# Performance work log

Hardware: AMD Instinct MI355X
Metric: run time of the kernel (lower is better)

## Reference

```python
import jax, jax.numpy as jnp
import numpy as np
from jax import lax

B, C, H, W = 32, 684, 16, 64
HID, A, CK, K = 256, 512, 512, 11


def setup_inputs() -> dict:
    key = jax.random.key(0)
    ks = jax.random.split(key, 12)
    s = 0.02
    return {
        "cnn_features": jax.random.normal(ks[0], (B, C, H, W), jnp.float32),
        "hidden": jax.random.normal(ks[1], (B, HID), jnp.float32),
        "alpha_sum": jax.random.uniform(ks[2], (B, 1, H, W), jnp.float32),
        "image_mask": jnp.ones((B, 1, H, W), jnp.float32),
        # hidden_weight: Linear(HID -> A)
        "Wh": jax.random.normal(ks[3], (A, HID), jnp.float32) * s,
        "bh": jnp.zeros((A,), jnp.float32),
        # encoder_feature_conv: Conv2d(C -> A, 1x1) == pointwise linear
        "Wec": jax.random.normal(ks[4], (A, C), jnp.float32) * s,
        "bec": jnp.zeros((A,), jnp.float32),
        # attention_conv: Conv2d(1 -> CK, 11x11, pad 5, no bias)
        "Wac": jax.random.normal(ks[5], (CK, 1, K, K), jnp.float32) * s,
        # attention_weight: Linear(CK -> A, no bias)
        "Waw": jax.random.normal(ks[6], (A, CK), jnp.float32) * s,
        # alpha_convert: Linear(A -> 1)
        "Wv": jax.random.normal(ks[7], (1, A), jnp.float32) * s,
        "bv": jnp.zeros((1,), jnp.float32),
    }


def reference(cnn_features, hidden, alpha_sum, image_mask,
              Wh, bh, Wec, bec, Wac, Waw, Wv, bv):
    # query = hidden_weight(hidden): [B, A]
    query = hidden @ Wh.T + bh
    # attention_conv(alpha_sum): [B, CK, H, W]
    ast = lax.conv_general_dilated(
        alpha_sum, Wac, window_strides=(1, 1),
        padding=[(K // 2, K // 2), (K // 2, K // 2)],
        dimension_numbers=("NCHW", "OIHW", "NCHW"))
    # attention_weight on permuted conv output: [B, H, W, A]
    coverage_alpha = jnp.einsum("bkhw,ak->bhwa", ast, Waw)
    # encoder_feature_conv (1x1 conv == pointwise linear): [B, H, W, A]
    cnn_trans = jnp.einsum("bchw,ac->bhwa", cnn_features, Wec) + bec
    # additive attention score
    alpha_score = jnp.tanh(query[:, None, None, :] + coverage_alpha + cnn_trans)
    # alpha_convert -> scalar energy per position: [B, H, W]
    energy = jnp.einsum("bhwa,a->bhw", alpha_score, Wv[0]) + bv[0]
    energy = energy - energy.max()  # global max-subtract as in original
    energy_exp = jnp.exp(energy) * image_mask[:, 0]
    denom = energy_exp.sum(axis=(-1, -2))[:, None, None] + 1e-10
    alpha = energy_exp / denom  # [B, H, W]
    alpha_sum_new = alpha[:, None, :, :] + alpha_sum  # [B, 1, H, W]
    # context: weighted spatial sum over features -> [B, C]
    context_vector = jnp.einsum("bhw,bchw->bc", alpha, cnn_features)
    return (context_vector, alpha, alpha_sum_new)
```

## Files before the change

kernel.cpp:

```cpp
#include <hip/hip_runtime.h>
#include <hip/hip_bf16.h>
#include <math.h>

#define Bn   32
#define Cn   684
#define Hn   16
#define Wn   64
#define HWn  1024
#define HIDn 256
#define An   512
#define KKn  121
#define CREAL 805
#define CPAD 832
#define NSTEP 26
#define NBLK 256

#define OUT_ALPHA 21888
#define OUT_ASUM  (21888 + 32768)

typedef short short8 __attribute__((ext_vector_type(8)));
typedef float floatx4 __attribute__((ext_vector_type(4)));

__device__ __forceinline__ unsigned short f2bf(float f) {
    union { float f; unsigned int i; } v; v.f = f;
    unsigned int i = v.i;
    return (unsigned short)((i + 0x7fffu + ((i >> 16) & 1u)) >> 16);
}
__device__ __forceinline__ unsigned int cvt2(float lo, float hi) {
    __hip_bfloat162 h = __float22bfloat162_rn(float2{lo, hi});
    union { __hip_bfloat162 h; unsigned int u; } cv; cv.h = h;
    return cv.u;
}

__device__ __forceinline__ size_t bfr_idx(int n, int k) {
    return ((((size_t)(n >> 4) * 26 + (k >> 5)) * 64
             + ((k >> 3) & 3) * 16 + (n & 15)) * 8) + (k & 7);
}

__global__ __launch_bounds__(256) void k_prep(
    const float* __restrict__ hidden,
    const float* __restrict__ Wh,
    const float* __restrict__ bh,
    const float* __restrict__ bec,
    const float* __restrict__ Wec,
    const float* __restrict__ Wac,
    const float* __restrict__ Waw,
    float* __restrict__ query,
    unsigned short* __restrict__ Bfr,
    float* __restrict__ energy)
{
    __shared__ float sbuf[512];
    const int blk = blockIdx.x, t = threadIdx.x;
    if (blk < 512) {
        const int a = blk;
        sbuf[t]       = Waw[(size_t)a * 512 + t];
        sbuf[t + 256] = Waw[(size_t)a * 512 + t + 256];
        __syncthreads();
        for (int cp = t; cp < Cn; cp += 256)
            Bfr[bfr_idx(a, cp)] = f2bf(Wec[(size_t)a * Cn + cp]);
        if (t < KKn) {
            float s = 0.f;
            #pragma unroll 8
            for (int k = 0; k < 512; ++k)
                s = fmaf(sbuf[k], Wac[k * KKn + t], s);
            Bfr[bfr_idx(a, Cn + t)] = f2bf(s);
        }
        for (int cp = CREAL + t; cp < CPAD; cp += 256)
            Bfr[bfr_idx(a, cp)] = 0;
    } else if (blk < 544) {
        const int b = blk - 512;
        sbuf[t] = (t < HIDn) ? hidden[b * HIDn + t] : 0.f;
        __syncthreads();
        for (int a = t; a < An; a += 256) {
            const float4* wp = (const float4*)(Wh + (size_t)a * HIDn);
            float s = bh[a] + bec[a];
            #pragma unroll 8
            for (int i = 0; i < HIDn / 4; ++i) {
                float4 w = wp[i];
                s = fmaf(sbuf[4 * i],     w.x, s);
                s = fmaf(sbuf[4 * i + 1], w.y, s);
                s = fmaf(sbuf[4 * i + 2], w.z, s);
                s = fmaf(sbuf[4 * i + 3], w.w, s);
            }
            query[b * An + a] = s;
        }
    } else {
        const int b = blk - 544;
        #pragma unroll
        for (int i = 0; i < 4; ++i)
            energy[b * HWn + i * 256 + t] = 0.f;
    }
}

__global__ __launch_bounds__(512, 4) void k_energy(
    const float* __restrict__ X,
    const float* __restrict__ asum,
    const float* __restrict__ Wv,
    const float* __restrict__ query,
    const unsigned short* __restrict__ Bfr,
    float* __restrict__ energy)
{
    __shared__ __align__(16) unsigned short As[2][64 * 40];
    __shared__ float plane[878];
    __shared__ int   lut[148];
    __shared__ float qs[NBLK];
    __shared__ float wvs[NBLK];
    __shared__ float red[8][64];

    const int t = threadIdx.x;
    const int d = blockIdx.x;
    const int nh  = (d >> 3) & 1;
    const int pid = (d >> 4) * 8 + (d & 7);
    const int hh = pid & 15, b = pid >> 4;
    const int w = t >> 6, lane = t & 63;
    const int q = lane >> 4, r = lane & 15;
    const int nbase = nh * NBLK;
    const int mA = lane;

    const float* Xb = X + (size_t)b * Cn * HWn + hh * Wn;
    const unsigned short* Bp = Bfr + (size_t)(nh * 16 + w * 2) * 26 * 512;

    for (int i = t; i < 878; i += 512) {
        float v = 0.f;
        if (i < 814) {
            int di = i / 74, cc = i - di * 74;
            int h2 = hh + di - 5, w2 = cc - 5;
            if (h2 >= 0 && h2 < Hn && w2 >= 0 && w2 < Wn)
                v = asum[b * HWn + h2 * Wn + w2];
        }
        plane[i] = v;
    }
    if (t < 148) {
        int off = 814;
        if (t < 121) { int di = t / 11; off = di * 74 + (t - di * 11); }
        lut[t] = off;
    }
    if (t < NBLK) {
        qs[t]  = query[b * An + nbase + t];
        wvs[t] = Wv[nbase + t];
    }
    {
        const float* xp = Xb + (size_t)(w * 4) * HWn + mA;
        float v0 = xp[0];
        float v1 = xp[(size_t)1 * HWn];
        float v2 = xp[(size_t)2 * HWn];
        float v3 = xp[(size_t)3 * HWn];
        *(uint2*)&As[0][mA * 40 + w * 4] = make_uint2(cvt2(v0, v1), cvt2(v2, v3));
    }
    __syncthreads();

    floatx4 acc[4][2];
    #pragma unroll
    for (int mf = 0; mf < 4; ++mf)
        #pragma unroll
        for (int nf = 0; nf < 2; ++nf)
            acc[mf][nf] = (floatx4){0.f, 0.f, 0.f, 0.f};

    for (int ch = 0; ch < NSTEP; ++ch) {
        const int cur = ch & 1;

        short8 bf[2];
        #pragma unroll
        for (int nf = 0; nf < 2; ++nf)
            bf[nf] = *(const short8*)(Bp + ((size_t)(nf * 26 + ch)) * 512 + lane * 8);

        short8 af[4];
        #pragma unroll
        for (int mf = 0; mf < 4; ++mf)
            af[mf] = *(const short8*)&As[cur][(mf * 16 + r) * 40 + q * 8];

        if (ch < NSTEP - 1) {
            const int c0 = (ch + 1) * 32 + w * 4;
            float va[4];
            #pragma unroll
            for (int j = 0; j < 4; ++j) {
                const int row = c0 + j;
                if (row < Cn) va[j] = Xb[(size_t)row * HWn + mA];
                else          va[j] = plane[lut[row - Cn] + mA];
            }
            *(uint2*)&As[cur ^ 1][mA * 40 + w * 4] =
                make_uint2(cvt2(va[0], va[1]), cvt2(va[2], va[3]));
        }

        #pragma unroll
        for (int mf = 0; mf < 4; ++mf)
            #pragma unroll
            for (int nf = 0; nf < 2; ++nf)
                acc[mf][nf] = __builtin_amdgcn_mfma_f32_16x16x32_bf16(
                    af[mf], bf[nf], acc[mf][nf], 0, 0, 0);

        __syncthreads();
    }

    float ep[16];
    #pragma unroll
    for (int i = 0; i < 16; ++i) ep[i] = 0.f;
    #pragma unroll
    for (int nf = 0; nf < 2; ++nf) {
        int nl = w * 32 + nf * 16 + r;
        float qv = qs[nl], wv = wvs[nl];
        #pragma unroll
        for (int mf = 0; mf < 4; ++mf)
            #pragma unroll
            for (int rg = 0; rg < 4; ++rg) {
                float x = acc[mf][nf][rg] + qv;
                float e2 = __expf(2.f * x);
                float th = 1.f - 2.f * __builtin_amdgcn_rcpf(e2 + 1.f);
                ep[mf * 4 + rg] += wv * th;
            }
    }
    #pragma unroll
    for (int i = 0; i < 16; ++i) {
        #pragma unroll
        for (int msk = 1; msk <= 8; msk <<= 1)
            ep[i] += __shfl_xor(ep[i], msk, 64);
    }
    if (r == 0) {
        #pragma unroll
        for (int mf = 0; mf < 4; ++mf)
            #pragma unroll
            for (int rg = 0; rg < 4; ++rg)
                red[w][mf * 16 + q * 4 + rg] = ep[mf * 4 + rg];
    }
    __syncthreads();
    if (t < 64) {
        float s = 0.f;
        #pragma unroll
        for (int ww = 0; ww < 8; ++ww) s += red[ww][t];
        atomicAdd(&energy[b * HWn + hh * Wn + t], s);
    }
}

__global__ __launch_bounds__(256) void k_softmax(
    const float* __restrict__ mask,
    const float* __restrict__ asum,
    float* __restrict__ energy,
    float* __restrict__ out)
{
    __shared__ float rsm[8];
    const int b = blockIdx.x;
    const int t = threadIdx.x, lane = t & 63, wid = t >> 6;

    float e[4], ex[4];
    #pragma unroll
    for (int i = 0; i < 4; ++i) e[i] = energy[b * HWn + i * 256 + t];
    float m = fmaxf(fmaxf(e[0], e[1]), fmaxf(e[2], e[3]));
    for (int off = 32; off >= 1; off >>= 1) m = fmaxf(m, __shfl_down(m, off, 64));
    if (lane == 0) rsm[wid] = m;
    __syncthreads();
    if (t == 0)
        rsm[4] = fmaxf(fmaxf(rsm[0], rsm[1]), fmaxf(rsm[2], rsm[3]));
    __syncthreads();
    const float M = rsm[4];
    float s = 0.f;
    #pragma unroll
    for (int i = 0; i < 4; ++i) {
        ex[i] = expf(e[i] - M) * mask[b * HWn + i * 256 + t];
        s += ex[i];
    }
    for (int off = 32; off >= 1; off >>= 1) s += __shfl_down(s, off, 64);
    __syncthreads();
    if (lane == 0) rsm[wid] = s;
    __syncthreads();
    if (t == 0) rsm[5] = rsm[0] + rsm[1] + rsm[2] + rsm[3] + 1e-10f;
    __syncthreads();
    const float denom = rsm[5];
    #pragma unroll
    for (int i = 0; i < 4; ++i) {
        int p = i * 256 + t;
        float a = ex[i] / denom;
        energy[b * HWn + p] = a;
        out[OUT_ALPHA + b * HWn + p] = a;
        out[OUT_ASUM  + b * HWn + p] = a + asum[b * HWn + p];
    }
}

__global__ __launch_bounds__(256) void k_ctx(
    const float* __restrict__ X,
    const float* __restrict__ alpha,
    float* __restrict__ out)
{
    __shared__ float al[1024];
    const int bx = blockIdx.x, b = blockIdx.y;
    const int t = threadIdx.x, lane = t & 63, wid = t >> 6;

    #pragma unroll
    for (int i = 0; i < 4; ++i) al[i * 256 + t] = alpha[b * HWn + i * 256 + t];
    __syncthreads();

    const int c = bx * 4 + wid;
    const float* xp = X + ((size_t)(b * Cn + c)) * HWn;
    float s2 = 0.f;
    #pragma unroll
    for (int i = 0; i < 4; ++i) {
        int off = i * 256 + lane * 4;
        float4 x = *(const float4*)(xp + off);
        float4 a = *(const float4*)(al + off);
        s2 = fmaf(a.x, x.x, s2);
        s2 = fmaf(a.y, x.y, s2);
        s2 = fmaf(a.z, x.z, s2);
        s2 = fmaf(a.w, x.w, s2);
    }
    for (int off = 32; off >= 1; off >>= 1) s2 += __shfl_down(s2, off, 64);
    if (lane == 0) out[b * Cn + c] = s2;
}

extern "C" void kernel_launch(void* const* d_in, const int* in_sizes, int n_in,
                              void* d_out, int out_size, void* d_ws, size_t ws_size,
                              hipStream_t stream)
{
    const float* X      = (const float*)d_in[0];
    const float* hidden = (const float*)d_in[1];
    const float* asum   = (const float*)d_in[2];
    const float* mask   = (const float*)d_in[3];
    const float* Wh     = (const float*)d_in[4];
    const float* bh     = (const float*)d_in[5];
    const float* Wec    = (const float*)d_in[6];
    const float* bec    = (const float*)d_in[7];
    const float* Wac    = (const float*)d_in[8];
    const float* Waw    = (const float*)d_in[9];
    const float* Wv     = (const float*)d_in[10];
    (void)in_sizes; (void)n_in; (void)out_size; (void)ws_size;

    float* out = (float*)d_out;
    float* ws = (float*)d_ws;
    float* query  = ws;
    float* energy = ws + 16384;
    unsigned short* Bfr = (unsigned short*)(ws + 16384 + 32768);

    k_prep    <<<dim3(576),      dim3(256), 0, stream>>>(hidden, Wh, bh, bec,
                                                         Wec, Wac, Waw, query, Bfr, energy);
    k_energy  <<<dim3(1024),     dim3(512), 0, stream>>>(X, asum, Wv, query, Bfr, energy);
    k_softmax <<<dim3(32),       dim3(256), 0, stream>>>(mask, asum, energy, out);
    k_ctx     <<<dim3(171, 32),  dim3(256), 0, stream>>>(X, energy, out);
}
```

Before: 238.3 us.

## Software-pipeline global loads two steps ahead in MFMA main loop

Restructures the K-loop into a two-stage unrolled pipeline. The B fragments and the next A-tile activations are prefetched into registers one to two steps ahead, so global load latency overlaps the MFMAs instead of stalling before each step. It also swaps __syncthreads for an explicit lgkmcnt wait plus s_barrier with sched_barriers to control scheduling. This raises register pressure and issues some redundant clamped loads at the tail.

```diff
diff --git a/kernel.cpp b/kernel.cpp
--- a/kernel.cpp
+++ b/kernel.cpp
@@ -147,6 +147,20 @@
         float v3 = xp[(size_t)3 * HWn];
         *(uint2*)&As[0][mA * 40 + w * 4] = make_uint2(cvt2(v0, v1), cvt2(v2, v3));
     }
+
+    short8 bfA[2], bfB[2];
+    float vaA[4], vaB[4];
+
+    #pragma unroll
+    for (int nf = 0; nf < 2; ++nf)
+        bfA[nf] = *(const short8*)(Bp + ((size_t)(nf * 26)) * 512 + lane * 8);
+    {
+        const float* xp = Xb + (size_t)(32 + w * 4) * HWn + mA;
+        vaA[0] = xp[0];
+        vaA[1] = xp[(size_t)1 * HWn];
+        vaA[2] = xp[(size_t)2 * HWn];
+        vaA[3] = xp[(size_t)3 * HWn];
+    }
     __syncthreads();
 
     floatx4 acc[4][2];
@@ -156,41 +170,74 @@
         for (int nf = 0; nf < 2; ++nf)
             acc[mf][nf] = (floatx4){0.f, 0.f, 0.f, 0.f};
 
-    for (int ch = 0; ch < NSTEP; ++ch) {
-        const int cur = ch & 1;
-
-        short8 bf[2];
-        #pragma unroll
-        for (int nf = 0; nf < 2; ++nf)
-            bf[nf] = *(const short8*)(Bp + ((size_t)(nf * 26 + ch)) * 512 + lane * 8);
-
-        short8 af[4];
-        #pragma unroll
-        for (int mf = 0; mf < 4; ++mf)
-            af[mf] = *(const short8*)&As[cur][(mf * 16 + r) * 40 + q * 8];
-
-        if (ch < NSTEP - 1) {
-            const int c0 = (ch + 1) * 32 + w * 4;
-            float va[4];
-            #pragma unroll
-            for (int j = 0; j < 4; ++j) {
-                const int row = c0 + j;
-                if (row < Cn) va[j] = Xb[(size_t)row * HWn + mA];
-                else          va[j] = plane[lut[row - Cn] + mA];
-            }
-            *(uint2*)&As[cur ^ 1][mA * 40 + w * 4] =
-                make_uint2(cvt2(va[0], va[1]), cvt2(va[2], va[3]));
-        }
-
-        #pragma unroll
-        for (int mf = 0; mf < 4; ++mf)
-            #pragma unroll
-            for (int nf = 0; nf < 2; ++nf)
-                acc[mf][nf] = __builtin_amdgcn_mfma_f32_16x16x32_bf16(
-                    af[mf], bf[nf], acc[mf][nf], 0, 0, 0);
-
-        __syncthreads();
-    }
+#define ISSUE_BF(DST, CC) {                                                   \
+    const int cb_ = (CC) <= 25 ? (CC) : 25;                                   \
+    _Pragma("unroll")                                                         \
+    for (int nf = 0; nf < 2; ++nf)                                            \
+        DST[nf] = *(const short8*)(Bp + ((size_t)(nf * 26 + cb_)) * 512       \
+                                      + lane * 8);                            \
+    }
+
+#define ISSUE_VA(DST, CC) {                                                   \
+    const int cc_ = (CC) <= 25 ? (CC) : 25;                                   \
+    const int c0_ = cc_ * 32 + w * 4;                                         \
+    _Pragma("unroll")                                                         \
+    for (int j = 0; j < 4; ++j) {                                             \
+        const int row = c0_ + j;                                              \
+        if (row < Cn) DST[j] = Xb[(size_t)row * HWn + mA];                    \
+        else          DST[j] = plane[lut[row - Cn] + mA];                     \
+    } }
+
+#define READA(CUR) {                                                          \
+    _Pragma("unroll")                                                         \
+    for (int mf = 0; mf < 4; ++mf)                                            \
+        af[mf] = *(const short8*)&As[CUR][(mf * 16 + r) * 40 + q * 8];        \
+    }
+
+#define MFMA8(BF) {                                                           \
+    _Pragma("unroll")                                                         \
+    for (int mf = 0; mf < 4; ++mf)                                            \
+        _Pragma("unroll")                                                     \
+        for (int nf = 0; nf < 2; ++nf)                                        \
+            acc[mf][nf] = __builtin_amdgcn_mfma_f32_16x16x32_bf16(            \
+                af[mf], BF[nf], acc[mf][nf], 0, 0, 0);                        \
+    }
+
+#define WRITEA(CUR, SRC) {                                                    \
+    *(uint2*)&As[CUR][mA * 40 + w * 4] =                                      \
+        make_uint2(cvt2(SRC[0], SRC[1]), cvt2(SRC[2], SRC[3]));               \
+    }
+
+#define LOOP_BARRIER() {                                                      \
+    asm volatile("s_waitcnt lgkmcnt(0)" ::: "memory");                        \
+    __builtin_amdgcn_sched_barrier(0);                                        \
+    __builtin_amdgcn_s_barrier();                                             \
+    __builtin_amdgcn_sched_barrier(0);                                        \
+    }
+
+    short8 af[4];
+    for (int ch = 0; ch < NSTEP; ch += 2) {
+        READA(0);
+        ISSUE_BF(bfB, ch + 1);
+        ISSUE_VA(vaB, ch + 2);
+        MFMA8(bfA);
+        WRITEA(1, vaA);
+        LOOP_BARRIER();
+
+        READA(1);
+        ISSUE_BF(bfA, ch + 2);
+        ISSUE_VA(vaA, ch + 3);
+        MFMA8(bfB);
+        if (ch + 2 < NSTEP) WRITEA(0, vaB);
+        LOOP_BARRIER();
+    }
+
+#undef ISSUE_BF
+#undef ISSUE_VA
+#undef READA
+#undef MFMA8
+#undef WRITEA
+#undef LOOP_BARRIER
 
     float ep[16];
     #pragma unroll
```

Result: no change. 240.3 us (+0.8%).
